# Performance work log

Measured on AMD Instinct MI355X. Metric: run time of the kernel, lower is better.

The kernel has to match this reference:

```python
import jax, jax.numpy as jnp
import numpy as np

B, S, H = 64, 2048, 512


def setup_inputs() -> dict:
    key = jax.random.key(0)
    k1, k2, k3, k4, k5 = jax.random.split(key, 5)
    scale = 1.0 / np.sqrt(H)
    return {
        "decoder_hidden": jax.random.normal(k1, (B, H), dtype=jnp.float32),
        "encoder_outputs": jax.random.normal(k2, (B, S, H), dtype=jnp.float32),
        "W_q": jax.random.normal(k3, (H, H), dtype=jnp.float32) * scale,
        "W_k": jax.random.normal(k4, (H, H), dtype=jnp.float32) * scale,
        "v": jax.random.normal(k5, (H,), dtype=jnp.float32) * scale,
    }


def reference(decoder_hidden, encoder_outputs, W_q, W_k, v):
    # query: [B,H] -> [B,1,H]; torch Linear computes x @ W.T
    query = (decoder_hidden @ W_q.T)[:, None, :]          # [B,1,H]
    keys = jnp.einsum('bsh,gh->bsg', encoder_outputs, W_k)  # [B,S,H]
    energy = jnp.tanh(query + keys)                        # [B,S,H]
    scores = jnp.einsum('bsh,h->bs', energy, v)            # [B,S]
    attention_weights = jax.nn.softmax(scores, axis=1)     # [B,S]
    context = jnp.einsum('bs,bsh->bh', attention_weights, encoder_outputs)
    return context, attention_weights
```

## Files before the change

kernel.cpp:

```cpp
#include <hip/hip_runtime.h>
#include <hip/hip_bf16.h>
#include <cstdint>


typedef __attribute__((ext_vector_type(8))) short short8;
typedef __attribute__((ext_vector_type(4))) float f32x4;

__device__ __forceinline__ unsigned short f2bf(float f) {
    unsigned u = __builtin_bit_cast(unsigned, f);
    u += 0x7FFFu + ((u >> 16) & 1u);
    return (unsigned short)(u >> 16);
}

__device__ __forceinline__ float tanh_fast(float x) {
    float e = __expf(2.0f * x);
    return 1.0f - 2.0f * __builtin_amdgcn_rcpf(e + 1.0f);
}

__device__ __forceinline__ void async16(const unsigned short* g, short* l) {
    __builtin_amdgcn_global_load_lds(
        (const __attribute__((address_space(1))) unsigned int*)g,
        (__attribute__((address_space(3))) unsigned int*)l, 16, 0, 0);
}

__global__ void cast_wk_kernel(const float* __restrict__ wk, unsigned short* __restrict__ wkb) {
    int i = (blockIdx.x * 256 + threadIdx.x) * 4;
    float4 f = *(const float4*)(wk + i);
    ushort4 o;
    o.x = f2bf(f.x); o.y = f2bf(f.y); o.z = f2bf(f.z); o.w = f2bf(f.w);
    *(ushort4*)(wkb + i) = o;
}

__global__ void q_kernel(const float* __restrict__ dec, const float* __restrict__ wq,
                         float* __restrict__ q) {
    int b  = blockIdx.x >> 3;
    int g0 = (blockIdx.x & 7) * 64;
    int t = threadIdx.x, lane = t & 63, w = t >> 6;
    __shared__ float dls[512];
    dls[t] = dec[b * 512 + t];
    dls[t + 256] = dec[b * 512 + 256 + t];
    __syncthreads();
    #pragma unroll
    for (int gi = 0; gi < 16; ++gi) {
        int g = g0 + w + gi * 4;
        float acc = 0.f;
        #pragma unroll
        for (int it = 0; it < 2; ++it) {
            int h = (it * 64 + lane) * 4;
            float4 wv = *(const float4*)(wq + (size_t)g * 512 + h);
            acc += wv.x * dls[h] + wv.y * dls[h + 1] + wv.z * dls[h + 2] + wv.w * dls[h + 3];
        }
        #pragma unroll
        for (int m = 32; m; m >>= 1) acc += __shfl_xor(acc, m, 64);
        if (lane == 0) q[b * 512 + g] = acc;
    }
}

__launch_bounds__(256, 2)
__global__ void scores_kernel(const float* __restrict__ enc, const unsigned short* __restrict__ wkb,
                              const float* __restrict__ q, const float* __restrict__ v,
                              float* __restrict__ scores) {
    __shared__ __align__(16) short Bs[512 * 32];
    __shared__ __align__(16) short As[64 * 40];
    __shared__ float q_s[512];
    __shared__ float v_s[512];
    __shared__ float red[4][64];

    int t = threadIdx.x, lane = t & 63, w = t >> 6;
    int quad = lane >> 4, l15 = lane & 15;
    int tile = blockIdx.x;
    int b = tile >> 5;
    size_t m0 = (size_t)tile * 64;

    q_s[t] = q[b * 512 + t];   q_s[t + 256] = q[b * 512 + 256 + t];
    v_s[t] = v[t];             v_s[t + 256] = v[t + 256];

    f32x4 acc[4][8];
    #pragma unroll
    for (int i = 0; i < 4; ++i)
        #pragma unroll
        for (int j = 0; j < 8; ++j)
            acc[i][j] = (f32x4){0.f, 0.f, 0.f, 0.f};

    int arow = t >> 2, akq = t & 3;
    const float* aptr = enc + (m0 + arow) * 512 + akq * 8;

    int kqs = (lane & 3) ^ ((lane >> 3) & 3);
    const unsigned short* bgbase = wkb + (size_t)(w * 16 + (lane >> 2)) * 512 + kqs * 8;
    short* blbase = &Bs[(w * 16 + (lane >> 2)) * 32 + (lane & 3) * 8];

    for (int kk = 0; kk < 512; kk += 32) {
        __syncthreads();
        #pragma unroll
        for (int i = 0; i < 8; ++i)
            async16(bgbase + (size_t)i * 64 * 512 + kk, blbase + i * 64 * 32);
        float4 fa0 = *(const float4*)(aptr + kk);
        float4 fa1 = *(const float4*)(aptr + kk + 4);
        short8 av;
        av[0] = (short)f2bf(fa0.x); av[1] = (short)f2bf(fa0.y);
        av[2] = (short)f2bf(fa0.z); av[3] = (short)f2bf(fa0.w);
        av[4] = (short)f2bf(fa1.x); av[5] = (short)f2bf(fa1.y);
        av[6] = (short)f2bf(fa1.z); av[7] = (short)f2bf(fa1.w);
        *(short8*)&As[arow * 40 + akq * 8] = av;
        __syncthreads();

        short8 af[4];
        #pragma unroll
        for (int mt = 0; mt < 4; ++mt)
            af[mt] = *(short8*)&As[(mt * 16 + l15) * 40 + quad * 8];
        #pragma unroll
        for (int nt = 0; nt < 8; ++nt) {
            int brow = w * 128 + nt * 16 + l15;
            short8 bf = *(short8*)&Bs[brow * 32 + (quad ^ ((l15 >> 1) & 3)) * 8];
            #pragma unroll
            for (int mt = 0; mt < 4; ++mt)
                acc[mt][nt] = __builtin_amdgcn_mfma_f32_16x16x32_bf16(af[mt], bf, acc[mt][nt], 0, 0, 0);
        }
    }

    float rs[4][4];
    #pragma unroll
    for (int mt = 0; mt < 4; ++mt)
        #pragma unroll
        for (int r = 0; r < 4; ++r) rs[mt][r] = 0.f;
    #pragma unroll
    for (int nt = 0; nt < 8; ++nt) {
        int g = w * 128 + nt * 16 + l15;
        float qb = q_s[g], vv = v_s[g];
        #pragma unroll
        for (int mt = 0; mt < 4; ++mt)
            #pragma unroll
            for (int r = 0; r < 4; ++r)
                rs[mt][r] += tanh_fast(qb + acc[mt][nt][r]) * vv;
    }
    #pragma unroll
    for (int m = 1; m <= 8; m <<= 1)
        #pragma unroll
        for (int mt = 0; mt < 4; ++mt)
            #pragma unroll
            for (int r = 0; r < 4; ++r)
                rs[mt][r] += __shfl_xor(rs[mt][r], m, 64);
    if (l15 == 0) {
        #pragma unroll
        for (int mt = 0; mt < 4; ++mt)
            #pragma unroll
            for (int r = 0; r < 4; ++r)
                red[w][mt * 16 + quad * 4 + r] = rs[mt][r];
    }
    __syncthreads();
    if (t < 64) {
        float sc = red[0][t] + red[1][t] + red[2][t] + red[3][t];
        scores[m0 + t] = sc;
    }
}

__global__ void softmax_kernel(float* __restrict__ out) {
    int b = blockIdx.x, t = threadIdx.x, lane = t & 63, w = t >> 6;
    float* sc = out + 32768 + b * 2048;
    __shared__ float wred[4];
    float vals[8];
    float mx = -1e30f;
    #pragma unroll
    for (int i = 0; i < 8; ++i) { vals[i] = sc[t + i * 256]; mx = fmaxf(mx, vals[i]); }
    #pragma unroll
    for (int m = 32; m; m >>= 1) mx = fmaxf(mx, __shfl_xor(mx, m, 64));
    if (lane == 0) wred[w] = mx;
    __syncthreads();
    mx = fmaxf(fmaxf(wred[0], wred[1]), fmaxf(wred[2], wred[3]));
    __syncthreads();
    float s = 0.f;
    #pragma unroll
    for (int i = 0; i < 8; ++i) { vals[i] = __expf(vals[i] - mx); s += vals[i]; }
    #pragma unroll
    for (int m = 32; m; m >>= 1) s += __shfl_xor(s, m, 64);
    if (lane == 0) wred[w] = s;
    __syncthreads();
    s = wred[0] + wred[1] + wred[2] + wred[3];
    float inv = 1.0f / s;
    #pragma unroll
    for (int i = 0; i < 8; ++i) sc[t + i * 256] = vals[i] * inv;
    out[b * 512 + t] = 0.f;
    out[b * 512 + 256 + t] = 0.f;
}

__launch_bounds__(256)
__global__ void context_kernel(const float* __restrict__ enc, float* __restrict__ out) {
    int blk = blockIdx.x;
    int b = blk >> 5, rem = blk & 31, hc = rem >> 4, ss = rem & 15;
    int t = threadIdx.x, lane = t & 63, sg = t >> 6;
    int h = hc * 256 + lane * 4;
    const float* wptr = out + 32768 + b * 2048;
    float ax = 0.f, ay = 0.f, az = 0.f, aw = 0.f;
    int sbase = ss * 128 + sg;
    #pragma unroll 8
    for (int i = 0; i < 32; ++i) {
        int s = sbase + i * 4;
        float wv = wptr[s];
        float4 e = *(const float4*)(enc + ((size_t)b * 2048 + s) * 512 + h);
        ax += wv * e.x; ay += wv * e.y; az += wv * e.z; aw += wv * e.w;
    }
    __shared__ float red[4][64][4];
    red[sg][lane][0] = ax; red[sg][lane][1] = ay; red[sg][lane][2] = az; red[sg][lane][3] = aw;
    __syncthreads();
    if (t < 64) {
        float* dst = out + b * 512 + hc * 256 + t * 4;
        #pragma unroll
        for (int j = 0; j < 4; ++j) {
            float sv = red[0][t][j] + red[1][t][j] + red[2][t][j] + red[3][t][j];
            atomicAdd(dst + j, sv);
        }
    }
}

extern "C" void kernel_launch(void* const* d_in, const int* in_sizes, int n_in,
                              void* d_out, int out_size, void* d_ws, size_t ws_size,
                              hipStream_t stream) {
    const float* dec = (const float*)d_in[0];
    const float* enc = (const float*)d_in[1];
    const float* wq  = (const float*)d_in[2];
    const float* wk  = (const float*)d_in[3];
    const float* v   = (const float*)d_in[4];
    float* out = (float*)d_out;

    unsigned short* wkb = (unsigned short*)d_ws;
    float* q = (float*)((char*)d_ws + 512 * 512 * 2);

    cast_wk_kernel<<<256, 256, 0, stream>>>(wk, wkb);
    q_kernel<<<512, 256, 0, stream>>>(dec, wq, q);
    scores_kernel<<<2048, 256, 0, stream>>>(enc, wkb, q, v, out + 32768);
    softmax_kernel<<<64, 256, 0, stream>>>(out);
    context_kernel<<<2048, 256, 0, stream>>>(enc, out);
}
```

Baseline: 470.2 us.

## Fuse context accumulation into scores kernel using unnormalized exp weights

Each scores block now computes exp(score) for its 64 rows and accumulates an unnormalized weighted sum of those encoder rows into a per-batch numerator buffer with atomics. The softmax kernel then rescales that numerator by exp(-max)/sum to produce the context. This removes the separate context kernel, which re-read the full encoder tensor from memory. The encoder tile should still be cache-resident from the GEMM. In exchange it adds global atomics, and it relies on scores being small enough that exp(score) cannot overflow without max subtraction.

```diff
diff --git a/kernel.cpp b/kernel.cpp
--- a/kernel.cpp
+++ b/kernel.cpp
@@ -23,12 +23,16 @@
         (__attribute__((address_space(3))) unsigned int*)l, 16, 0, 0);
 }
 
-__global__ void cast_wk_kernel(const float* __restrict__ wk, unsigned short* __restrict__ wkb) {
+__global__ void cast_wk_kernel(const float* __restrict__ wk, unsigned short* __restrict__ wkb,
+                               float* __restrict__ numer) {
     int i = (blockIdx.x * 256 + threadIdx.x) * 4;
     float4 f = *(const float4*)(wk + i);
     ushort4 o;
     o.x = f2bf(f.x); o.y = f2bf(f.y); o.z = f2bf(f.z); o.w = f2bf(f.w);
     *(ushort4*)(wkb + i) = o;
+    if (blockIdx.x < 32) {
+        *(float4*)(numer + i) = (float4){0.f, 0.f, 0.f, 0.f};
+    }
 }
 
 __global__ void q_kernel(const float* __restrict__ dec, const float* __restrict__ wq,
@@ -59,12 +63,13 @@
 __launch_bounds__(256, 2)
 __global__ void scores_kernel(const float* __restrict__ enc, const unsigned short* __restrict__ wkb,
                               const float* __restrict__ q, const float* __restrict__ v,
-                              float* __restrict__ scores) {
+                              float* __restrict__ scores, float* __restrict__ numer) {
     __shared__ __align__(16) short Bs[512 * 32];
     __shared__ __align__(16) short As[64 * 40];
     __shared__ float q_s[512];
     __shared__ float v_s[512];
     __shared__ float red[4][64];
+    __shared__ float w_lds[64];
 
     int t = threadIdx.x, lane = t & 63, w = t >> 6;
     int quad = lane >> 4, l15 = lane & 15;
@@ -151,10 +156,26 @@
     if (t < 64) {
         float sc = red[0][t] + red[1][t] + red[2][t] + red[3][t];
         scores[m0 + t] = sc;
-    }
-}
-
-__global__ void softmax_kernel(float* __restrict__ out) {
+        w_lds[t] = __expf(sc);
+    }
+    __syncthreads();
+
+    {
+        float n0 = 0.f, n1 = 0.f;
+        const float* ep = enc + m0 * 512 + t * 2;
+        #pragma unroll 16
+        for (int s = 0; s < 64; ++s) {
+            float wv = w_lds[s];
+            float2 e = *(const float2*)(ep + (size_t)s * 512);
+            n0 += wv * e.x; n1 += wv * e.y;
+        }
+        float* np = numer + b * 512 + t * 2;
+        atomicAdd(np, n0);
+        atomicAdd(np + 1, n1);
+    }
+}
+
+__global__ void softmax_kernel(float* __restrict__ out, const float* __restrict__ numer) {
     int b = blockIdx.x, t = threadIdx.x, lane = t & 63, w = t >> 6;
     float* sc = out + 32768 + b * 2048;
     __shared__ float wred[4];
@@ -179,37 +200,9 @@
     float inv = 1.0f / s;
     #pragma unroll
     for (int i = 0; i < 8; ++i) sc[t + i * 256] = vals[i] * inv;
-    out[b * 512 + t] = 0.f;
-    out[b * 512 + 256 + t] = 0.f;
-}
-
-__launch_bounds__(256)
-__global__ void context_kernel(const float* __restrict__ enc, float* __restrict__ out) {
-    int blk = blockIdx.x;
-    int b = blk >> 5, rem = blk & 31, hc = rem >> 4, ss = rem & 15;
-    int t = threadIdx.x, lane = t & 63, sg = t >> 6;
-    int h = hc * 256 + lane * 4;
-    const float* wptr = out + 32768 + b * 2048;
-    float ax = 0.f, ay = 0.f, az = 0.f, aw = 0.f;
-    int sbase = ss * 128 + sg;
-    #pragma unroll 8
-    for (int i = 0; i < 32; ++i) {
-        int s = sbase + i * 4;
-        float wv = wptr[s];
-        float4 e = *(const float4*)(enc + ((size_t)b * 2048 + s) * 512 + h);
-        ax += wv * e.x; ay += wv * e.y; az += wv * e.z; aw += wv * e.w;
-    }
-    __shared__ float red[4][64][4];
-    red[sg][lane][0] = ax; red[sg][lane][1] = ay; red[sg][lane][2] = az; red[sg][lane][3] = aw;
-    __syncthreads();
-    if (t < 64) {
-        float* dst = out + b * 512 + hc * 256 + t * 4;
-        #pragma unroll
-        for (int j = 0; j < 4; ++j) {
-            float sv = red[0][t][j] + red[1][t][j] + red[2][t][j] + red[3][t][j];
-            atomicAdd(dst + j, sv);
-        }
-    }
+    float csc = __expf(-mx) * inv;
+    out[b * 512 + t]       = numer[b * 512 + t] * csc;
+    out[b * 512 + 256 + t] = numer[b * 512 + 256 + t] * csc;
 }
 
 extern "C" void kernel_launch(void* const* d_in, const int* in_sizes, int n_in,
@@ -224,10 +217,10 @@
 
     unsigned short* wkb = (unsigned short*)d_ws;
     float* q = (float*)((char*)d_ws + 512 * 512 * 2);
-
-    cast_wk_kernel<<<256, 256, 0, stream>>>(wk, wkb);
+    float* numer = (float*)((char*)d_ws + 512 * 512 * 2 + 64 * 512 * 4);
+
+    cast_wk_kernel<<<256, 256, 0, stream>>>(wk, wkb, numer);
     q_kernel<<<512, 256, 0, stream>>>(dec, wq, q);
-    scores_kernel<<<2048, 256, 0, stream>>>(enc, wkb, q, v, out + 32768);
-    softmax_kernel<<<64, 256, 0, stream>>>(out);
-    context_kernel<<<2048, 256, 0, stream>>>(enc, out);
-}
+    scores_kernel<<<2048, 256, 0, stream>>>(enc, wkb, q, v, out + 32768, numer);
+    softmax_kernel<<<64, 256, 0, stream>>>(out, numer);
+}
```

Result: faster. 452.5 us (-3.8%).
